# Kernel optimization log

Measured on AMD Instinct MI355X. Metric: run time of the kernel, lower is better.

## Reference

```python
import jax, jax.numpy as jnp
import numpy as np

N_QUBITS = 4


def _apply_ry(state, theta, wire):
    """Apply RY(theta) on `wire`. state: (B,2,2,2,2) real; theta: (B,) or scalar."""
    ax = wire + 1
    half = theta * 0.5
    c, s = jnp.cos(half), jnp.sin(half)
    a0 = jax.lax.index_in_dim(state, 0, axis=ax, keepdims=False)
    a1 = jax.lax.index_in_dim(state, 1, axis=ax, keepdims=False)
    if c.ndim:  # per-sample angles -> broadcast over remaining qubit axes
        c = c.reshape((-1,) + (1,) * (a0.ndim - 1))
        s = s.reshape((-1,) + (1,) * (a0.ndim - 1))
    n0 = c * a0 - s * a1
    n1 = s * a0 + c * a1
    return jnp.stack([n0, n1], axis=ax)


def _apply_cnot(state, control, target):
    """CNOT on the (B,2,2,2,2) statevector: flip target where control==1."""
    cax = control + 1
    s0 = jax.lax.index_in_dim(state, 0, axis=cax, keepdims=False)
    s1 = jax.lax.index_in_dim(state, 1, axis=cax, keepdims=False)
    # after removing the control axis, axes after it shift down by one
    tax = target + 1 if target < control else target
    s1 = jnp.flip(s1, axis=tax)
    return jnp.stack([s0, s1], axis=cax)


def _circuit(x, weights):
    """Batched 4-qubit circuit. x: (B,4) angles; weights: (3,4). Returns (B,4) <Z_i>."""
    B = x.shape[0]
    state = jnp.zeros((B, 2, 2, 2, 2), dtype=x.dtype).at[:, 0, 0, 0, 0].set(1.0)
    for i in range(N_QUBITS):
        state = _apply_ry(state, x[:, i], i)
    for layer in range(3):
        for i in range(N_QUBITS):
            state = _apply_ry(state, weights[layer, i], i)
        if layer < 2:  # CNOT ring between RY layers
            for i in range(3):
                state = _apply_cnot(state, i, i + 1)
            state = _apply_cnot(state, 3, 0)
    probs = state * state  # real statevector -> |amp|^2
    expvals = []
    for w in range(N_QUBITS):
        other = tuple(a for a in range(1, N_QUBITS + 1) if a != w + 1)
        p = probs.sum(axis=other)  # (B,2)
        expvals.append(p[:, 0] - p[:, 1])
    return jnp.stack(expvals, axis=1)  # (B,4)


def setup_inputs() -> dict:
    key = jax.random.key(0)
    k1, k2, k3, k4 = jax.random.split(key, 4)
    B = 1_000_000
    return {
        "x": jax.random.normal(k1, (B, 4), dtype=jnp.float32),
        "quantum_weights": jax.random.normal(k2, (3, 4), dtype=jnp.float32),
        "W": jax.random.normal(k3, (6, 4), dtype=jnp.float32) * 0.5,
        "b": jax.random.normal(k4, (6,), dtype=jnp.float32) * 0.1,
    }


def reference(x, quantum_weights, W, b):
    q_out = _circuit(x, quantum_weights)          # (B,4)
    logits = q_out @ W.T + b                      # Linear(4,6)
    return jax.nn.softmax(logits, axis=1)         # (B,6)
```

## Files before the change

### kernel.cpp

```cpp
#include <hip/hip_runtime.h>


#define INV_2PI 0.15915494309189535f

template <int MASK>
__device__ __forceinline__ void apply_ry(float st[16], float c, float s) {
#pragma unroll
    for (int i = 0; i < 16; ++i) {
        if (!(i & MASK)) {
            float a0 = st[i];
            float a1 = st[i | MASK];
            st[i]        = fmaf(c, a0, -s * a1);
            st[i | MASK] = fmaf(s, a0,  c * a1);
        }
    }
}

template <int CMASK, int TMASK>
__device__ __forceinline__ void apply_cnot(float st[16]) {
#pragma unroll
    for (int i = 0; i < 16; ++i) {
        if ((i & CMASK) && !(i & TMASK)) {
            float tmp     = st[i];
            st[i]         = st[i | TMASK];
            st[i | TMASK] = tmp;
        }
    }
}

__global__ __launch_bounds__(256) void qnn_kernel(
    const float* __restrict__ x,
    const float* __restrict__ qw,
    const float* __restrict__ W,
    const float* __restrict__ bias,
    float* __restrict__ out,
    int B)
{
    __shared__ float wc[12], ws[12];
    __shared__ float sW[24], sb[6];

    const int tid = threadIdx.x;
    if (tid < 12) {
        float r = qw[tid] * (0.5f * INV_2PI);
        wc[tid] = __builtin_amdgcn_cosf(r);
        ws[tid] = __builtin_amdgcn_sinf(r);
    }
    if (tid < 24) sW[tid] = W[tid];
    if (tid < 6)  sb[tid] = bias[tid];
    __syncthreads();

    const int b = blockIdx.x * 256 + tid;
    if (b >= B) return;

    const float4 xv = reinterpret_cast<const float4*>(x)[b];

    float c0, s0, c1, s1, c2, s2, c3, s3;
    {
        float r0 = xv.x * (0.5f * INV_2PI);
        float r1 = xv.y * (0.5f * INV_2PI);
        float r2 = xv.z * (0.5f * INV_2PI);
        float r3 = xv.w * (0.5f * INV_2PI);
        c0 = __builtin_amdgcn_cosf(r0); s0 = __builtin_amdgcn_sinf(r0);
        c1 = __builtin_amdgcn_cosf(r1); s1 = __builtin_amdgcn_sinf(r1);
        c2 = __builtin_amdgcn_cosf(r2); s2 = __builtin_amdgcn_sinf(r2);
        c3 = __builtin_amdgcn_cosf(r3); s3 = __builtin_amdgcn_sinf(r3);
    }

    float a01[4] = { c0 * c1, c0 * s1, s0 * c1, s0 * s1 };
    float a23[4] = { c2 * c3, c2 * s3, s2 * c3, s2 * s3 };

    float st[16];
#pragma unroll
    for (int hi = 0; hi < 4; ++hi)
#pragma unroll
        for (int lo = 0; lo < 4; ++lo)
            st[hi * 4 + lo] = a01[hi] * a23[lo];

#pragma unroll
    for (int l = 0; l < 3; ++l) {
        apply_ry<8>(st, wc[l * 4 + 0], ws[l * 4 + 0]);
        apply_ry<4>(st, wc[l * 4 + 1], ws[l * 4 + 1]);
        apply_ry<2>(st, wc[l * 4 + 2], ws[l * 4 + 2]);
        apply_ry<1>(st, wc[l * 4 + 3], ws[l * 4 + 3]);
        if (l < 2) {
            apply_cnot<8, 4>(st);
            apply_cnot<4, 2>(st);
            apply_cnot<2, 1>(st);
            apply_cnot<1, 8>(st);
        }
    }

    float p[16];
#pragma unroll
    for (int i = 0; i < 16; ++i) p[i] = st[i] * st[i];

    float z[4];
#pragma unroll
    for (int w = 0; w < 4; ++w) {
        const int m = 8 >> w;
        float sum = 0.0f;
#pragma unroll
        for (int i = 0; i < 16; ++i)
            if (i & m) sum += p[i];
        z[w] = fmaf(-2.0f, sum, 1.0f);
    }

    float e[6];
    float sum = 0.0f;
#pragma unroll
    for (int j = 0; j < 6; ++j) {
        float a = sb[j];
        a = fmaf(z[0], sW[j * 4 + 0], a);
        a = fmaf(z[1], sW[j * 4 + 1], a);
        a = fmaf(z[2], sW[j * 4 + 2], a);
        a = fmaf(z[3], sW[j * 4 + 3], a);
        e[j] = __expf(a);
        sum += e[j];
    }
    const float inv = __builtin_amdgcn_rcpf(sum);

    float2* o2 = reinterpret_cast<float2*>(out + (size_t)b * 6);
    o2[0] = make_float2(e[0] * inv, e[1] * inv);
    o2[1] = make_float2(e[2] * inv, e[3] * inv);
    o2[2] = make_float2(e[4] * inv, e[5] * inv);
}

extern "C" void kernel_launch(void* const* d_in, const int* in_sizes, int n_in,
                              void* d_out, int out_size, void* d_ws, size_t ws_size,
                              hipStream_t stream) {
    const float* x    = (const float*)d_in[0];
    const float* qw   = (const float*)d_in[1];
    const float* W    = (const float*)d_in[2];
    const float* bias = (const float*)d_in[3];
    float* out = (float*)d_out;

    const int B = in_sizes[0] / 4;
    const int blocks = (B + 255) / 256;
    qnn_kernel<<<blocks, 256, 0, stream>>>(x, qw, W, bias, out, B);
}
```

Measured before the change: 85.95 us.

## Fold first and last RY layers algebraically and stage output through LDS

Merges the first weight RY layer into the input angle RY, since both act on a product state and their angles add. The last RY layer is folded into the Z expectation by combining cos/sin of the full angle with a cross-term sum. This removes two full RY layers of per-thread arithmetic. Results are also staged in shared memory so the block writes its outputs as coalesced float4 stores instead of strided float2 stores, at the cost of a second barrier and 6 KB of LDS per block.

```diff
diff --git a/kernel.cpp b/kernel.cpp
--- a/kernel.cpp
+++ b/kernel.cpp
@@ -36,30 +36,38 @@
     float* __restrict__ out,
     int B)
 {
-    __shared__ float wc[12], ws[12];
+    __shared__ float qw0[4];
+    __shared__ float c1h[4], s1h[4];
+    __shared__ float c2f[4], s2f[4];
     __shared__ float sW[24], sb[6];
+    __shared__ float so[256 * 6];
 
     const int tid = threadIdx.x;
-    if (tid < 12) {
-        float r = qw[tid] * (0.5f * INV_2PI);
-        wc[tid] = __builtin_amdgcn_cosf(r);
-        ws[tid] = __builtin_amdgcn_sinf(r);
+    if (tid < 4) {
+        qw0[tid] = qw[tid];
+        float r1 = qw[4 + tid] * (0.5f * INV_2PI);
+        c1h[tid] = __builtin_amdgcn_cosf(r1);
+        s1h[tid] = __builtin_amdgcn_sinf(r1);
+        float r2 = qw[8 + tid] * INV_2PI;
+        c2f[tid] = __builtin_amdgcn_cosf(r2);
+        s2f[tid] = __builtin_amdgcn_sinf(r2);
     }
     if (tid < 24) sW[tid] = W[tid];
     if (tid < 6)  sb[tid] = bias[tid];
     __syncthreads();
 
     const int b = blockIdx.x * 256 + tid;
-    if (b >= B) return;
+    const bool valid = (b < B);
 
-    const float4 xv = reinterpret_cast<const float4*>(x)[b];
+    float4 xv = valid ? reinterpret_cast<const float4*>(x)[b]
+                      : make_float4(0.f, 0.f, 0.f, 0.f);
 
     float c0, s0, c1, s1, c2, s2, c3, s3;
     {
-        float r0 = xv.x * (0.5f * INV_2PI);
-        float r1 = xv.y * (0.5f * INV_2PI);
-        float r2 = xv.z * (0.5f * INV_2PI);
-        float r3 = xv.w * (0.5f * INV_2PI);
+        float r0 = (xv.x + qw0[0]) * (0.5f * INV_2PI);
+        float r1 = (xv.y + qw0[1]) * (0.5f * INV_2PI);
+        float r2 = (xv.z + qw0[2]) * (0.5f * INV_2PI);
+        float r3 = (xv.w + qw0[3]) * (0.5f * INV_2PI);
         c0 = __builtin_amdgcn_cosf(r0); s0 = __builtin_amdgcn_sinf(r0);
         c1 = __builtin_amdgcn_cosf(r1); s1 = __builtin_amdgcn_sinf(r1);
         c2 = __builtin_amdgcn_cosf(r2); s2 = __builtin_amdgcn_sinf(r2);
@@ -76,19 +84,16 @@
         for (int lo = 0; lo < 4; ++lo)
             st[hi * 4 + lo] = a01[hi] * a23[lo];
 
-#pragma unroll
-    for (int l = 0; l < 3; ++l) {
-        apply_ry<8>(st, wc[l * 4 + 0], ws[l * 4 + 0]);
-        apply_ry<4>(st, wc[l * 4 + 1], ws[l * 4 + 1]);
-        apply_ry<2>(st, wc[l * 4 + 2], ws[l * 4 + 2]);
-        apply_ry<1>(st, wc[l * 4 + 3], ws[l * 4 + 3]);
-        if (l < 2) {
-            apply_cnot<8, 4>(st);
-            apply_cnot<4, 2>(st);
-            apply_cnot<2, 1>(st);
-            apply_cnot<1, 8>(st);
-        }
-    }
+    apply_cnot<8, 4>(st); apply_cnot<4, 2>(st);
+    apply_cnot<2, 1>(st); apply_cnot<1, 8>(st);
+
+    apply_ry<8>(st, c1h[0], s1h[0]);
+    apply_ry<4>(st, c1h[1], s1h[1]);
+    apply_ry<2>(st, c1h[2], s1h[2]);
+    apply_ry<1>(st, c1h[3], s1h[3]);
+
+    apply_cnot<8, 4>(st); apply_cnot<4, 2>(st);
+    apply_cnot<2, 1>(st); apply_cnot<1, 8>(st);
 
     float p[16];
 #pragma unroll
@@ -98,11 +103,15 @@
 #pragma unroll
     for (int w = 0; w < 4; ++w) {
         const int m = 8 >> w;
-        float sum = 0.0f;
+        float A1 = 0.0f, X = 0.0f;
 #pragma unroll
-        for (int i = 0; i < 16; ++i)
-            if (i & m) sum += p[i];
-        z[w] = fmaf(-2.0f, sum, 1.0f);
+        for (int i = 0; i < 16; ++i) {
+            if (!(i & m)) {
+                A1 += p[i | m];
+                X  = fmaf(st[i], st[i | m], X);
+            }
+        }
+        z[w] = fmaf(c2f[w], fmaf(-2.0f, A1, 1.0f), -2.0f * s2f[w] * X);
     }
 
     float e[6];
@@ -119,10 +128,20 @@
     }
     const float inv = __builtin_amdgcn_rcpf(sum);
 
-    float2* o2 = reinterpret_cast<float2*>(out + (size_t)b * 6);
-    o2[0] = make_float2(e[0] * inv, e[1] * inv);
-    o2[1] = make_float2(e[2] * inv, e[3] * inv);
-    o2[2] = make_float2(e[4] * inv, e[5] * inv);
+#pragma unroll
+    for (int j = 0; j < 6; ++j) so[tid * 6 + j] = e[j] * inv;
+    __syncthreads();
+
+    const float4* so4 = reinterpret_cast<const float4*>(so);
+    float4* out4 = reinterpret_cast<float4*>(out);
+    const long long base = (long long)blockIdx.x * 384;
+    const long long total4 = (long long)B * 6 / 4;
+#pragma unroll
+    for (int k = 0; k < 2; ++k) {
+        int idx = tid + k * 256;
+        if (idx < 384 && base + idx < total4)
+            out4[base + idx] = so4[idx];
+    }
 }
 
 extern "C" void kernel_launch(void* const* d_in, const int* in_sizes, int n_in,
```

Result: faster. 81.08 us (median of 2 runs) (-5.7%).
